# Performance work log

Hardware: AMD Instinct MI355X
Metric: run time of the kernel (lower is better)

## Reference

```python
import jax, jax.numpy as jnp
import numpy as np

USER_NUM = 100000
ITEM_NUM = 100000
DIM = 64
BS = 256


def setup_inputs() -> dict:
    key = jax.random.key(0)
    k1, k2, k3, k4, k5 = jax.random.split(key, 5)
    # xavier_normal-ish scale for embeddings/linear
    user_table = jax.random.normal(k1, (USER_NUM, DIM), dtype=jnp.float32) * 0.1
    item_table = jax.random.normal(k2, (ITEM_NUM, DIM), dtype=jnp.float32) * 0.1
    cls_w = jax.random.normal(k3, (5, DIM), dtype=jnp.float32) * (2.0 / (DIM + 5)) ** 0.5
    cls_b = jnp.zeros((5,), dtype=jnp.float32)
    batch_user = jax.random.randint(k4, (BS,), 0, USER_NUM, dtype=jnp.int64)
    values = jnp.array([[1.0, 2.0, 3.0, 4.0, 5.0]], dtype=jnp.float32)
    return {
        "batch_user": batch_user,
        "user_table": user_table,
        "item_table": item_table,
        "cls_w": cls_w,
        "cls_b": cls_b,
        "values": values,
    }


def reference(batch_user, user_table, item_table, cls_w, cls_b, values):
    # forward_full_items: score every (user, item) pair.
    # Torch materializes h_ui = (u repeated) * (items tiled) of shape
    # [bs*item_num, dim]; mathematically logits = einsum over dim, so we
    # fuse the broadcasted product with the tiny Linear to avoid the
    # huge expanded intermediate while computing identical math.
    u = user_table[batch_user]                       # [bs, dim]
    # logits[b,i,c] = sum_d u[b,d] * item[i,d] * W[c,d] + b[c]
    logits = jnp.einsum('bd,id,cd->bic', u, item_table, cls_w) + cls_b  # [bs, item_num, 5]
    prob = jax.nn.softmax(logits, axis=-1)
    return jnp.sum(prob * values[0], axis=-1)        # [bs, item_num]
```

## Files before the change

kernel.cpp:

```cpp
#include <hip/hip_runtime.h>

#define I_TOTAL 100000
#define DIM 64
#define BS 256

typedef __attribute__((ext_vector_type(8))) short bf16x8;
typedef __attribute__((ext_vector_type(4))) float f32x4;

__device__ inline unsigned short f2bf(float x) {
    union { float f; unsigned u; } v; v.f = x;
    return (unsigned short)((v.u + 0x8000u) >> 16);
}

__device__ inline unsigned pk_bf16(float lo, float hi) {
    unsigned r;
    asm("v_cvt_pk_bf16_f32 %0, %1, %2" : "=v"(r) : "v"(lo), "v"(hi));
    return r;
}

__device__ inline bf16x8 pack8(float4 a, float4 b) {
    union { unsigned u[4]; bf16x8 v; } r;
    r.u[0] = pk_bf16(a.x, a.y);
    r.u[1] = pk_bf16(a.z, a.w);
    r.u[2] = pk_bf16(b.x, b.y);
    r.u[3] = pk_bf16(b.z, b.w);
    return r.v;
}

__device__ inline float rfl(float x) {
    union { float f; int i; } u; u.f = x;
    u.i = __builtin_amdgcn_readfirstlane(u.i);
    return u.f;
}

__global__ __launch_bounds__(256) void conv_items(
    const float* __restrict__ item, unsigned short* __restrict__ itbf)
{
    long t = (long)blockIdx.x * 256 + threadIdx.x;
    const float4* p = (const float4*)(item + t * 8);
    float4 a = p[0], b = p[1];
    ushort4 r0, r1;
    r0.x = f2bf(a.x); r0.y = f2bf(a.y); r0.z = f2bf(a.z); r0.w = f2bf(a.w);
    r1.x = f2bf(b.x); r1.y = f2bf(b.y); r1.z = f2bf(b.z); r1.w = f2bf(b.w);
    ushort4* q = (ushort4*)(itbf + t * 8);
    q[0] = r0; q[1] = r1;
}

__device__ inline void mfma_tile_sw(const bf16x8 (&afr)[5][2], bf16x8 b0, bf16x8 b1,
                                    f32x4 (&acc)[5])
{
    const f32x4 zero = (f32x4){0.f, 0.f, 0.f, 0.f};
#pragma unroll
    for (int c = 0; c < 5; ++c) {
        acc[c] = __builtin_amdgcn_mfma_f32_16x16x32_bf16(b0, afr[c][0], zero, 0, 0, 0);
        acc[c] = __builtin_amdgcn_mfma_f32_16x16x32_bf16(b1, afr[c][1], acc[c], 0, 0, 0);
    }
}

__device__ inline f32x4 softmax_vec(const f32x4 (&acc)[5], const float (&sw)[5],
                                    const float (&swv)[5])
{
    f32x4 r;
#pragma unroll
    for (int rr = 0; rr < 4; ++rr) {
        float e0 = __builtin_amdgcn_exp2f(acc[0][rr]);
        float e1 = __builtin_amdgcn_exp2f(acc[1][rr]);
        float e2 = __builtin_amdgcn_exp2f(acc[2][rr]);
        float e3 = __builtin_amdgcn_exp2f(acc[3][rr]);
        float e4 = __builtin_amdgcn_exp2f(acc[4][rr]);
        float den = e0 * sw[0];
        den = fmaf(e1, sw[1], den);
        den = fmaf(e2, sw[2], den);
        den = fmaf(e3, sw[3], den);
        den = fmaf(e4, sw[4], den);
        float num = e0 * swv[0];
        num = fmaf(e1, swv[1], num);
        num = fmaf(e2, swv[2], num);
        num = fmaf(e3, swv[3], num);
        num = fmaf(e4, swv[4], num);
        r[rr] = num * __builtin_amdgcn_rcpf(den);
    }
    return r;
}

__global__ __launch_bounds__(64) void gemm_softmax(
    const unsigned short* __restrict__ itbf,
    const int* __restrict__ bu, const float* __restrict__ ut,
    const float* __restrict__ cw, const float* __restrict__ clsb,
    const float* __restrict__ vals, float* __restrict__ out)
{
    const int blk  = blockIdx.x;
    const int r8   = blk & 7;
    const int rest = blk >> 3;
    const int wv   = rest & 3;
    const int qq   = rest >> 2;
    const int g    = qq & 15;
    const int a    = qq >> 4;
    const int y    = a * 8 + r8;
    if (y >= 98) return;

    const int lane = threadIdx.x & 63;
    const int col  = lane & 15;
    const int quad = lane >> 4;

    const int b_base = g * 16;
    const int i_base = y * 1024 + wv * 256;
    if (i_base >= I_TOTAL) return;

    const float s = 1.4426950408889634f;

    const float* up = ut + (size_t)bu[b_base + col] * DIM + quad * 8;
    float4 u0 = *(const float4*)(up);
    float4 u1 = *(const float4*)(up + 4);
    float4 u2 = *(const float4*)(up + 32);
    float4 u3 = *(const float4*)(up + 36);
    u0.x *= s; u0.y *= s; u0.z *= s; u0.w *= s;
    u1.x *= s; u1.y *= s; u1.z *= s; u1.w *= s;
    u2.x *= s; u2.y *= s; u2.z *= s; u2.w *= s;
    u3.x *= s; u3.y *= s; u3.z *= s; u3.w *= s;

    bf16x8 afr[5][2];
    float sw[5], swv[5];
#pragma unroll
    for (int c = 0; c < 5; ++c) {
        const float* wp = cw + c * DIM + quad * 8;
        float4 w0 = *(const float4*)(wp);
        float4 w1 = *(const float4*)(wp + 4);
        float4 w2 = *(const float4*)(wp + 32);
        float4 w3 = *(const float4*)(wp + 36);
        float4 m0 = make_float4(u0.x*w0.x, u0.y*w0.y, u0.z*w0.z, u0.w*w0.w);
        float4 m1 = make_float4(u1.x*w1.x, u1.y*w1.y, u1.z*w1.z, u1.w*w1.w);
        float4 m2 = make_float4(u2.x*w2.x, u2.y*w2.y, u2.z*w2.z, u2.w*w2.w);
        float4 m3 = make_float4(u3.x*w3.x, u3.y*w3.y, u3.z*w3.z, u3.w*w3.w);
        afr[c][0] = pack8(m0, m1);
        afr[c][1] = pack8(m2, m3);
        float w = __builtin_amdgcn_exp2f(clsb[c] * s);
        sw[c]  = rfl(w);
        swv[c] = rfl(w * vals[c]);
    }

    const unsigned short* bp = itbf + (size_t)(i_base + col) * DIM + quad * 8;
    float* op = out + (size_t)(b_base + col) * I_TOTAL + i_base + quad * 4;

    if (i_base + 256 <= I_TOTAL) {
#pragma unroll 2
        for (int t = 0; t < 16; ++t) {
            bf16x8 b0 = *(const bf16x8*)(bp + t * 1024);
            bf16x8 b1 = *(const bf16x8*)(bp + t * 1024 + 32);
            f32x4 acc[5];
            mfma_tile_sw(afr, b0, b1, acc);
            f32x4 r = softmax_vec(acc, sw, swv);
            __builtin_nontemporal_store(r, (f32x4*)(op + t * 16));
        }
    } else {
#pragma unroll 1
        for (int t = 0; t < 16; ++t) {
            if (i_base + t * 16 >= I_TOTAL) break;
            int irow = i_base + t * 16 + col;
            int ic = irow < I_TOTAL ? irow : I_TOTAL - 1;
            const unsigned short* p2 = itbf + (size_t)ic * DIM + quad * 8;
            bf16x8 b0 = *(const bf16x8*)p2;
            bf16x8 b1 = *(const bf16x8*)(p2 + 32);
            f32x4 acc[5];
            mfma_tile_sw(afr, b0, b1, acc);
            f32x4 r = softmax_vec(acc, sw, swv);
            int ie = i_base + t * 16 + quad * 4;
#pragma unroll
            for (int rr = 0; rr < 4; ++rr) {
                if (ie + rr < I_TOTAL)
                    out[(size_t)(b_base + col) * I_TOTAL + ie + rr] = r[rr];
            }
        }
    }
}

__global__ __launch_bounds__(64) void gemm_softmax_fb(
    const int* __restrict__ bu, const float* __restrict__ ut,
    const float* __restrict__ it, const float* __restrict__ cw,
    const float* __restrict__ clsb, const float* __restrict__ vals,
    float* __restrict__ out)
{
    const int blk  = blockIdx.x;
    const int r8   = blk & 7;
    const int rest = blk >> 3;
    const int wv   = rest & 3;
    const int qq   = rest >> 2;
    const int g    = qq & 15;
    const int a    = qq >> 4;
    const int y    = a * 8 + r8;
    if (y >= 98) return;

    const int lane = threadIdx.x & 63;
    const int col  = lane & 15;
    const int quad = lane >> 4;

    const int b_base = g * 16;
    const int i_base = y * 1024 + wv * 256;
    if (i_base >= I_TOTAL) return;

    const float s = 1.4426950408889634f;

    const float* up = ut + (size_t)bu[b_base + col] * DIM + quad * 8;
    float4 u0 = *(const float4*)(up);
    float4 u1 = *(const float4*)(up + 4);
    float4 u2 = *(const float4*)(up + 32);
    float4 u3 = *(const float4*)(up + 36);
    u0.x *= s; u0.y *= s; u0.z *= s; u0.w *= s;
    u1.x *= s; u1.y *= s; u1.z *= s; u1.w *= s;
    u2.x *= s; u2.y *= s; u2.z *= s; u2.w *= s;
    u3.x *= s; u3.y *= s; u3.z *= s; u3.w *= s;

    bf16x8 afr[5][2];
    float sw[5], swv[5];
#pragma unroll
    for (int c = 0; c < 5; ++c) {
        const float* wp = cw + c * DIM + quad * 8;
        float4 w0 = *(const float4*)(wp);
        float4 w1 = *(const float4*)(wp + 4);
        float4 w2 = *(const float4*)(wp + 32);
        float4 w3 = *(const float4*)(wp + 36);
        float4 m0 = make_float4(u0.x*w0.x, u0.y*w0.y, u0.z*w0.z, u0.w*w0.w);
        float4 m1 = make_float4(u1.x*w1.x, u1.y*w1.y, u1.z*w1.z, u1.w*w1.w);
        float4 m2 = make_float4(u2.x*w2.x, u2.y*w2.y, u2.z*w2.z, u2.w*w2.w);
        float4 m3 = make_float4(u3.x*w3.x, u3.y*w3.y, u3.z*w3.z, u3.w*w3.w);
        afr[c][0] = pack8(m0, m1);
        afr[c][1] = pack8(m2, m3);
        float w = __builtin_amdgcn_exp2f(clsb[c] * s);
        sw[c]  = rfl(w);
        swv[c] = rfl(w * vals[c]);
    }

#pragma unroll 1
    for (int t = 0; t < 16; ++t) {
        if (i_base + t * 16 >= I_TOTAL) break;
        int irow = i_base + t * 16 + col;
        int ic = irow < I_TOTAL ? irow : I_TOTAL - 1;
        const float* p2 = it + (size_t)ic * DIM + quad * 8;
        float4 q0 = *(const float4*)(p2);
        float4 q1 = *(const float4*)(p2 + 4);
        float4 q2 = *(const float4*)(p2 + 32);
        float4 q3 = *(const float4*)(p2 + 36);
        bf16x8 b0 = pack8(q0, q1);
        bf16x8 b1 = pack8(q2, q3);
        f32x4 acc[5];
        mfma_tile_sw(afr, b0, b1, acc);
        f32x4 r = softmax_vec(acc, sw, swv);
        int ie = i_base + t * 16 + quad * 4;
        if (ie + 4 <= I_TOTAL) {
            __builtin_nontemporal_store(r,
                (f32x4*)(out + (size_t)(b_base + col) * I_TOTAL + ie));
        } else {
#pragma unroll
            for (int rr = 0; rr < 4; ++rr)
                if (ie + rr < I_TOTAL)
                    out[(size_t)(b_base + col) * I_TOTAL + ie + rr] = r[rr];
        }
    }
}

extern "C" void kernel_launch(void* const* d_in, const int* in_sizes, int n_in,
                              void* d_out, int out_size, void* d_ws, size_t ws_size,
                              hipStream_t stream) {
    const int*   bu   = (const int*)d_in[0];
    const float* ut   = (const float*)d_in[1];
    const float* it   = (const float*)d_in[2];
    const float* cw   = (const float*)d_in[3];
    const float* cb   = (const float*)d_in[4];
    const float* vals = (const float*)d_in[5];
    float* out = (float*)d_out;
    unsigned short* itbf = (unsigned short*)d_ws;

    const size_t needed = (size_t)I_TOTAL * DIM * 2;

    if (ws_size >= needed) {
        conv_items<<<3125, 256, 0, stream>>>(it, itbf);
        gemm_softmax<<<6656, 64, 0, stream>>>(itbf, bu, ut, cw, cb, vals, out);
    } else {
        gemm_softmax_fb<<<6656, 64, 0, stream>>>(bu, ut, it, cw, cb, vals, out);
    }
}
```

Before: 175.1 us.

## Triple-buffer item tile loads with inline asm and manual vmcnt waits

```diff
diff --git a/kernel.cpp b/kernel.cpp
--- a/kernel.cpp
+++ b/kernel.cpp
@@ -109,6 +109,30 @@
 
     const float s = 1.4426950408889634f;
 
+    const unsigned short* bp = itbf + (size_t)(i_base + col) * DIM + quad * 8;
+    const bool fast = (i_base + 256 <= I_TOTAL);
+
+#define LOADT(T, R0w, R1w) do {                                               \
+    unsigned long long la0 = (unsigned long long)(bp + (size_t)(T) * 1024);   \
+    unsigned long long la1 = la0 + 64;                                        \
+    asm volatile("global_load_dwordx4 %0, %1, off"                            \
+                 : "=&v"(R0w) : "v"(la0) : "memory");                         \
+    asm volatile("global_load_dwordx4 %0, %1, off"                            \
+                 : "=&v"(R1w) : "v"(la1) : "memory");                         \
+} while (0)
+
+#define WAITN(NW) do {                                                        \
+    asm volatile("s_waitcnt vmcnt(" #NW ")" ::: "memory");                    \
+    __builtin_amdgcn_sched_barrier(0);                                        \
+} while (0)
+
+    bf16x8 sA0, sA1, sB0, sB1, sC0, sC1;
+    if (fast) {
+        LOADT(0, sA0, sA1);
+        LOADT(1, sB0, sB1);
+        LOADT(2, sC0, sC1);
+    }
+
     const float* up = ut + (size_t)bu[b_base + col] * DIM + quad * 8;
     float4 u0 = *(const float4*)(up);
     float4 u1 = *(const float4*)(up + 4);
@@ -139,19 +163,51 @@
         swv[c] = rfl(w * vals[c]);
     }
 
-    const unsigned short* bp = itbf + (size_t)(i_base + col) * DIM + quad * 8;
     float* op = out + (size_t)(b_base + col) * I_TOTAL + i_base + quad * 4;
 
-    if (i_base + 256 <= I_TOTAL) {
-#pragma unroll 2
-        for (int t = 0; t < 16; ++t) {
-            bf16x8 b0 = *(const bf16x8*)(bp + t * 1024);
-            bf16x8 b1 = *(const bf16x8*)(bp + t * 1024 + 32);
-            f32x4 acc[5];
-            mfma_tile_sw(afr, b0, b1, acc);
-            f32x4 r = softmax_vec(acc, sw, swv);
-            __builtin_nontemporal_store(r, (f32x4*)(op + t * 16));
-        }
+    if (fast) {
+#define STORET(T, R) do {                                                     \
+    unsigned long long ad = (unsigned long long)(op + (T) * 16);              \
+    asm volatile("global_store_dwordx4 %0, %1, off"                           \
+                 :: "v"(ad), "v"(R) : "memory");                              \
+} while (0)
+
+#define ROUND_L(T, NW, S0, S1) do {                                           \
+    WAITN(NW);                                                                \
+    f32x4 acc[5];                                                             \
+    mfma_tile_sw(afr, S0, S1, acc);                                           \
+    LOADT((T) + 3, S0, S1);                                                   \
+    f32x4 r = softmax_vec(acc, sw, swv);                                      \
+    STORET(T, r);                                                             \
+} while (0)
+
+#define ROUND_N(T, NW, S0, S1) do {                                           \
+    WAITN(NW);                                                                \
+    f32x4 acc[5];                                                             \
+    mfma_tile_sw(afr, S0, S1, acc);                                           \
+    f32x4 r = softmax_vec(acc, sw, swv);                                      \
+    STORET(T, r);                                                             \
+} while (0)
+
+        ROUND_L(0,  4, sA0, sA1);
+        ROUND_L(1,  5, sB0, sB1);
+        ROUND_L(2,  6, sC0, sC1);
+        ROUND_L(3,  7, sA0, sA1);
+        ROUND_L(4,  7, sB0, sB1);
+        ROUND_L(5,  7, sC0, sC1);
+        ROUND_L(6,  7, sA0, sA1);
+        ROUND_L(7,  7, sB0, sB1);
+        ROUND_L(8,  7, sC0, sC1);
+        ROUND_L(9,  7, sA0, sA1);
+        ROUND_L(10, 7, sB0, sB1);
+        ROUND_L(11, 7, sC0, sC1);
+        ROUND_L(12, 7, sA0, sA1);
+        ROUND_N(13, 7, sB0, sB1);
+        ROUND_N(14, 5, sC0, sC1);
+        ROUND_N(15, 3, sA0, sA1);
+#undef ROUND_L
+#undef ROUND_N
+#undef STORET
     } else {
 #pragma unroll 1
         for (int t = 0; t < 16; ++t) {
@@ -172,6 +228,8 @@
             }
         }
     }
+#undef LOADT
+#undef WAITN
 }
 
 __global__ __launch_bounds__(64) void gemm_softmax_fb(
@@ -247,8 +305,7 @@
         f32x4 r = softmax_vec(acc, sw, swv);
         int ie = i_base + t * 16 + quad * 4;
         if (ie + 4 <= I_TOTAL) {
-            __builtin_nontemporal_store(r,
-                (f32x4*)(out + (size_t)(b_base + col) * I_TOTAL + ie));
+            *(f32x4*)(out + (size_t)(b_base + col) * I_TOTAL + ie) = r;
         } else {
 #pragma unroll
             for (int rr = 0; rr < 4; ++rr)
```

Measured after the change: 172.1 us. Within noise of the previous version (-1.7%).
